# Kernel tuning notes

Measured on AMD Instinct MI355X. Metric: run time of the kernel, lower is better.

## Reference

```python
import jax, jax.numpy as jnp
import numpy as np

B, T, F, U, L, C = 1024, 100, 300, 512, 2, 10
EPS = 1e-3  # keras LayerNormalization default epsilon


def _ln(z, g, b):
    m = jnp.mean(z, axis=-1, keepdims=True)
    v = jnp.var(z, axis=-1, keepdims=True)
    return (z - m) * jax.lax.rsqrt(v + EPS) * g + b


def _cell(xt, h, c, W, R, bias, kg, kb, rg, rb, sg, sb):
    # LayerNormLSTMCell: LN(x@W) + LN(h@R) + b, gates i,f,g,o; LN on new cell state
    z = _ln(xt @ W, kg, kb) + _ln(h @ R, rg, rb) + bias
    i, f, g, o = jnp.split(z, 4, axis=-1)
    c_new = jax.nn.sigmoid(f) * c + jax.nn.sigmoid(i) * jnp.tanh(g)
    c_new = _ln(c_new, sg, sb)
    h_new = jax.nn.sigmoid(o) * jnp.tanh(c_new)
    return h_new, c_new


def setup_inputs() -> dict:
    key = jax.random.key(0)
    ks = jax.random.split(key, 8 + 2 * L)
    d = {}
    d["x"] = jax.random.normal(ks[0], (B, T, F), jnp.float32)
    lens = jax.random.randint(ks[1], (B,), 1, T + 1)
    d["mask"] = (jnp.arange(T)[None, :] < lens[:, None]).astype(jnp.int32)
    in_dims = [F, U]
    ki = 2
    for l in range(L):
        s = 1.0 / np.sqrt(in_dims[l])
        d[f"W{l}"] = jax.random.uniform(ks[ki], (in_dims[l], 4 * U), jnp.float32, -s, s); ki += 1
        d[f"R{l}"] = jax.random.uniform(ks[ki], (U, 4 * U), jnp.float32, -0.044, 0.044); ki += 1
        d[f"b{l}"] = jnp.zeros((4 * U,), jnp.float32)
        d[f"kg{l}"] = jnp.ones((4 * U,), jnp.float32)
        d[f"kb{l}"] = jnp.zeros((4 * U,), jnp.float32)
        d[f"rg{l}"] = jnp.ones((4 * U,), jnp.float32)
        d[f"rb{l}"] = jnp.zeros((4 * U,), jnp.float32)
        d[f"sg{l}"] = jnp.ones((U,), jnp.float32)
        d[f"sb{l}"] = jnp.zeros((U,), jnp.float32)
    s = 1.0 / np.sqrt(U)
    d["Wd"] = jax.random.uniform(ks[ki], (U, C), jnp.float32, -s, s)
    d["bd"] = jnp.zeros((C,), jnp.float32)
    return d


def _forward(x, mask,
             W0, R0, b0, kg0, kb0, rg0, rb0, sg0, sb0,
             W1, R1, b1, kg1, kb1, rg1, rb1, sg1, sb1,
             Wd, bd):
    params = [
        (W0, R0, b0, kg0, kb0, rg0, rb0, sg0, sb0),
        (W1, R1, b1, kg1, kb1, rg1, rb1, sg1, sb1),
    ]
    bsz = x.shape[0]
    dt = x.dtype

    def step(carry, inp_t):
        states, out_prev = carry
        xt, mt = inp_t  # xt: [B,F], mt: [B] bool
        mb = mt[:, None]
        inp = xt
        new_states = []
        for (h, c), p in zip(states, params):
            hn, cn = _cell(inp, h, c, *p)
            inp = hn
            # Keras RNN masking: carry previous state at masked steps
            new_states.append((jnp.where(mb, hn, h), jnp.where(mb, cn, c)))
        out = jnp.where(mb, inp, out_prev)
        return (tuple(new_states), out), None

    init_states = tuple((jnp.zeros((bsz, U), dt), jnp.zeros((bsz, U), dt)) for _ in range(L))
    carry0 = (init_states, jnp.zeros((bsz, U), dt))
    xs = (jnp.transpose(x, (1, 0, 2)), mask.T.astype(bool))  # time-major
    (_, out), _ = jax.lax.scan(step, carry0, xs)
    return jax.nn.softmax(out @ Wd + bd, axis=-1)


def reference(x, mask,
              W0, R0, b0, kg0, kb0, rg0, rb0, sg0, sb0,
              W1, R1, b1, kg1, kb1, rg1, rb1, sg1, sb1,
              Wd, bd):
    return _forward(x, mask,
                    W0, R0, b0, kg0, kb0, rg0, rb0, sg0, sb0,
                    W1, R1, b1, kg1, kb1, rg1, rb1, sg1, sb1,
                    Wd, bd)
```

## Files before the change

kernel.cpp:

```cpp
#include <hip/hip_runtime.h>

#define B_ 1024
#define T_ 100
#define F_ 300
#define FP_ 320
#define U_ 512
#define G4_ 2048
#define C_ 10
#define EPS_ 1e-3f

typedef _Float16 f16x8 __attribute__((ext_vector_type(8)));
typedef float f32x4 __attribute__((ext_vector_type(4)));

typedef __attribute__((address_space(1))) const void* gcptr_t;
typedef __attribute__((address_space(3))) void* lptr_t;

__device__ __forceinline__ void async_ld16(_Float16* lds, const _Float16* g) {
  __builtin_amdgcn_global_load_lds((gcptr_t)g, (lptr_t)lds, 16, 0, 0);
}

__global__ __launch_bounds__(1024) void prep_kernel(const int* __restrict__ mask,
                                                    int* __restrict__ perm,
                                                    int* __restrict__ nt) {
  __shared__ int cnt[T_ + 1];
  __shared__ int start[T_ + 1];
  int b = threadIdx.x;
  if (b <= T_) cnt[b] = 0;
  __syncthreads();
  const int* mrow = mask + (size_t)b * T_;
  int len = 0;
  for (int t = 0; t < T_; t++) len += mrow[t];
  atomicAdd(&cnt[len], 1);
  __syncthreads();
  if (b == 0) {
    int run = 0;
    for (int l = T_; l >= 0; l--) {
      start[l] = run;
      run += cnt[l];
    }
  }
  __syncthreads();
  if (b < T_) nt[b] = start[b];
  __syncthreads();
  int pos = atomicAdd(&start[len], 1);
  perm[pos] = b;
}


__global__ __launch_bounds__(256) void cast_x_kernel(const float* __restrict__ x,
                                                     const int* __restrict__ perm,
                                                     const int* __restrict__ nt,
                                                     _Float16* __restrict__ xhi,
                                                     _Float16* __restrict__ xlo) {
  size_t cidx = (size_t)blockIdx.x * 256 + threadIdx.x;
  int fc = (int)(cidx % (FP_ / 8));
  size_t bt = cidx / (FP_ / 8);
  int i = (int)(bt % B_);
  int t = (int)(bt / B_);
  int nr = (nt[t] + 127) & ~127;
  if (i >= nr) return;
  int b = perm[i];
  int f = fc * 8;
  const float* xr = x + ((size_t)b * T_ + t) * F_;
  float v[8];
  if (f + 8 <= F_) {
    float4 a = *(const float4*)(xr + f);
    float4 c = *(const float4*)(xr + f + 4);
    v[0] = a.x; v[1] = a.y; v[2] = a.z; v[3] = a.w;
    v[4] = c.x; v[5] = c.y; v[6] = c.z; v[7] = c.w;
  } else {
#pragma unroll
    for (int j = 0; j < 8; j++) v[j] = (f + j < F_) ? xr[f + j] : 0.f;
  }
  f16x8 hi, lo;
#pragma unroll
  for (int j = 0; j < 8; j++) {
    _Float16 h = (_Float16)v[j];
    hi[j] = h;
    lo[j] = (_Float16)(v[j] - (float)h);
  }
  *(f16x8*)(xhi + cidx * 8) = hi;
  *(f16x8*)(xlo + cidx * 8) = lo;
}

__global__ __launch_bounds__(256) void cast_w_kernel(const float* __restrict__ W,
                                                     _Float16* __restrict__ Whi,
                                                     _Float16* __restrict__ Wlo,
                                                     int K, int N, int Kp) {
  __shared__ float tile[32][33];
  int n0 = blockIdx.x * 32, k0 = blockIdx.y * 32;
  int tx = threadIdx.x & 31, ty = threadIdx.x >> 5;
#pragma unroll
  for (int r = 0; r < 32; r += 8) {
    int k = k0 + ty + r;
    tile[ty + r][tx] = (k < K) ? W[(size_t)k * N + n0 + tx] : 0.f;
  }
  __syncthreads();
#pragma unroll
  for (int r = 0; r < 32; r += 8) {
    int n = n0 + ty + r, kk = k0 + tx;
    if (kk < Kp) {
      float v = tile[tx][ty + r];
      _Float16 h = (_Float16)v;
      Whi[(size_t)n * Kp + kk] = h;
      Wlo[(size_t)n * Kp + kk] = (_Float16)(v - (float)h);
    }
  }
}

struct GemmOp {
  const _Float16* A;
  const _Float16* Bt;
  float* G;
  int lda;
  int K;
  size_t aLo;
  int step;
};
struct G4Pack {
  GemmOp op[4];
  const int* nt;
};

__global__ __launch_bounds__(512, 1) void gemm_phase(G4Pack P) {
  GemmOp op = P.op[blockIdx.z];
  const int mBase = blockIdx.y * 128, nBase = blockIdx.x * 128;
  if (mBase >= P.nt[op.step]) return;
  const int K = op.K, lda = op.lda;
  const _Float16* Ah = op.A;
  const _Float16* Al = op.A + op.aLo;
  const _Float16* Bh = op.Bt;
  const _Float16* Bl = op.Bt + (size_t)G4_ * K;

  __shared__ __align__(16) _Float16 lds[2][4][128 * 64];

  const int tid = threadIdx.x;
  const int w = tid >> 6;
  const int lane = tid & 63;
  const int wm = (w & 1) << 6;
  const int wn = (w >> 1) << 5;

  f32x4 acc[4][2];
#pragma unroll
  for (int mt = 0; mt < 4; mt++)
#pragma unroll
    for (int nt2 = 0; nt2 < 2; nt2++) acc[mt][nt2] = (f32x4){0.f, 0.f, 0.f, 0.f};

  const int i0 = w << 1;

#define STAGE(BUF, K0)                                                    \
  do {                                                                    \
    _Float16* base_ = &lds[BUF][0][0];                                    \
    _Pragma("unroll") for (int j = 0; j < 2; j++) {                       \
      int i = i0 + j;                                                     \
      int idx = (i << 6) + lane;                                          \
      int row = idx >> 3;                                                 \
      int cl = ((idx & 7) ^ (row & 7)) << 3;                              \
      size_t aoff = (size_t)(mBase + row) * lda + (K0) + cl;              \
      size_t boff = (size_t)(nBase + row) * K + (K0) + cl;                \
      async_ld16(base_ + (i << 9), Ah + aoff);                            \
      async_ld16(base_ + 8192 + (i << 9), Al + aoff);                     \
      async_ld16(base_ + 16384 + (i << 9), Bh + boff);                    \
      async_ld16(base_ + 24576 + (i << 9), Bl + boff);                    \
    }                                                                     \
  } while (0)

  STAGE(0, 0);
  __syncthreads();

  const int nch = K >> 6;
  int cur = 0;
#pragma unroll 1
  for (int c = 0; c < nch; c++) {
    if (c + 1 < nch) STAGE(cur ^ 1, (c + 1) << 6);
    const _Float16* ash = &lds[cur][0][0];
    const _Float16* asl = &lds[cur][1][0];
    const _Float16* bsh = &lds[cur][2][0];
    const _Float16* bsl = &lds[cur][3][0];
#pragma unroll
    for (int q = 0; q < 2; q++) {
      f16x8 afh[4], afl[4], bfh[2], bfl[2];
#pragma unroll
      for (int mt = 0; mt < 4; mt++) {
        int row = wm + (mt << 4) + (lane & 15);
        int p = ((q << 2) + (lane >> 4)) ^ (row & 7);
        afh[mt] = *(const f16x8*)&ash[(row << 6) + (p << 3)];
        afl[mt] = *(const f16x8*)&asl[(row << 6) + (p << 3)];
      }
#pragma unroll
      for (int nt2 = 0; nt2 < 2; nt2++) {
        int row = wn + (nt2 << 4) + (lane & 15);
        int p = ((q << 2) + (lane >> 4)) ^ (row & 7);
        bfh[nt2] = *(const f16x8*)&bsh[(row << 6) + (p << 3)];
        bfl[nt2] = *(const f16x8*)&bsl[(row << 6) + (p << 3)];
      }
      __builtin_amdgcn_s_setprio(1);
#pragma unroll
      for (int mt = 0; mt < 4; mt++)
#pragma unroll
        for (int nt2 = 0; nt2 < 2; nt2++) {
          acc[mt][nt2] = __builtin_amdgcn_mfma_f32_16x16x32_f16(afh[mt], bfh[nt2], acc[mt][nt2], 0, 0, 0);
          acc[mt][nt2] = __builtin_amdgcn_mfma_f32_16x16x32_f16(afl[mt], bfh[nt2], acc[mt][nt2], 0, 0, 0);
          acc[mt][nt2] = __builtin_amdgcn_mfma_f32_16x16x32_f16(afh[mt], bfl[nt2], acc[mt][nt2], 0, 0, 0);
        }
      __builtin_amdgcn_s_setprio(0);
    }
    __syncthreads();
    cur ^= 1;
  }
#undef STAGE

  int q4 = lane >> 4, cc = lane & 15;
  float* G = op.G;
#pragma unroll
  for (int mt = 0; mt < 4; mt++)
#pragma unroll
    for (int nt2 = 0; nt2 < 2; nt2++)
#pragma unroll
      for (int r = 0; r < 4; r++) {
        int row = mBase + wm + (mt << 4) + (q4 << 2) + r;
        int col = nBase + wn + (nt2 << 4) + cc;
        G[(size_t)row * G4_ + col] = acc[mt][nt2][r];
      }
}


__device__ __forceinline__ void block_reduce(float* v, int n, float* sred, int tid) {
  int lane = tid & 63, w = tid >> 6;
  for (int off = 32; off > 0; off >>= 1)
    for (int i = 0; i < n; i++) v[i] += __shfl_down(v[i], off, 64);
  if (lane == 0)
    for (int i = 0; i < n; i++) sred[w * 4 + i] = v[i];
  __syncthreads();
  if (tid == 0)
    for (int i = 0; i < n; i++) sred[16 + i] = sred[i] + sred[4 + i] + sred[8 + i] + sred[12 + i];
  __syncthreads();
  for (int i = 0; i < n; i++) v[i] = sred[16 + i];
}

__device__ __forceinline__ float sigm(float x) { return 1.f / (1.f + expf(-x)); }

struct CellOp {
  const float* Gx;
  const float* Gh;
  const float* bias;
  const float* kg;
  const float* kb;
  const float* rg;
  const float* rb;
  const float* sg;
  const float* sb;
  float* cS;
  _Float16* hP;
  float* outb;
  int step;
};
struct C2Pack {
  CellOp op[2];
  const int* nt;
};

__global__ __launch_bounds__(256) void cell_phase(C2Pack P) {
  CellOp cp = P.op[blockIdx.x >> 10];
  int b = blockIdx.x & (B_ - 1);
  if (b >= P.nt[cp.step]) return;
  int tid = threadIdx.x;
  __shared__ float sred[20];
  const float* gx = cp.Gx + (size_t)b * G4_;
  const float* gh = cp.Gh + (size_t)b * G4_;
  float vx[8], vh[8];
  float s[4] = {0.f, 0.f, 0.f, 0.f};
#pragma unroll
  for (int i = 0; i < 8; i++) {
    int col = tid + (i << 8);
    float a = gx[col], d = gh[col];
    vx[i] = a;
    vh[i] = d;
    s[0] += a;
    s[1] += a * a;
    s[2] += d;
    s[3] += d * d;
  }
  block_reduce(s, 4, sred, tid);
  const float inv = 1.f / 2048.f;
  float m1 = s[0] * inv, m2 = s[2] * inv;
  float rs1 = rsqrtf(fmaxf(s[1] * inv - m1 * m1, 0.f) + EPS_);
  float rs2 = rsqrtf(fmaxf(s[3] * inv - m2 * m2, 0.f) + EPS_);
  float z[8];
#pragma unroll
  for (int i = 0; i < 8; i++) {
    int col = tid + (i << 8);
    z[i] = (vx[i] - m1) * rs1 * cp.kg[col] + cp.kb[col] +
           (vh[i] - m2) * rs2 * cp.rg[col] + cp.rb[col] + cp.bias[col];
  }
  int j0 = tid, j1 = tid + 256;
  size_t base = (size_t)b * U_;
  _Float16* hHi = cp.hP;
  _Float16* hLo = cp.hP + (size_t)B_ * U_;
  float co0 = cp.cS[base + j0], co1 = cp.cS[base + j1];
  float cn0 = sigm(z[2]) * co0 + sigm(z[0]) * tanhf(z[4]);
  float cn1 = sigm(z[3]) * co1 + sigm(z[1]) * tanhf(z[5]);
  float t2[2] = {cn0 + cn1, cn0 * cn0 + cn1 * cn1};
  block_reduce(t2, 2, sred, tid);
  const float invU = 1.f / 512.f;
  float mc = t2[0] * invU;
  float rsc = rsqrtf(fmaxf(t2[1] * invU - mc * mc, 0.f) + EPS_);
  float cl0 = (cn0 - mc) * rsc * cp.sg[j0] + cp.sb[j0];
  float cl1 = (cn1 - mc) * rsc * cp.sg[j1] + cp.sb[j1];
  float hn0 = sigm(z[6]) * tanhf(cl0);
  float hn1 = sigm(z[7]) * tanhf(cl1);
  _Float16 hh0 = (_Float16)hn0, hh1 = (_Float16)hn1;
  hHi[base + j0] = hh0;
  hLo[base + j0] = (_Float16)(hn0 - (float)hh0);
  hHi[base + j1] = hh1;
  hLo[base + j1] = (_Float16)(hn1 - (float)hh1);
  cp.cS[base + j0] = cl0;
  cp.cS[base + j1] = cl1;
  if (cp.outb) {
    cp.outb[base + j0] = hn0;
    cp.outb[base + j1] = hn1;
  }
}

__global__ __launch_bounds__(64) void dense_softmax_kernel(const float* __restrict__ outb,
                                                           const float* __restrict__ Wd,
                                                           const float* __restrict__ bd,
                                                           const int* __restrict__ perm,
                                                           float* __restrict__ o) {
  int b = blockIdx.x, lane = threadIdx.x;
  __shared__ float sl[16];
  int col = lane & 15, kg = lane >> 4;
  float acc = 0.f;
  if (col < C_) {
    for (int k = kg; k < U_; k += 4) acc += outb[(size_t)b * U_ + k] * Wd[(size_t)k * C_ + col];
  }
  acc += __shfl_down(acc, 16, 64);
  acc += __shfl_down(acc, 32, 64);
  if (lane < C_) sl[lane] = acc + bd[lane];
  __syncthreads();
  if (lane < C_) {
    float mx = sl[0];
    for (int i = 1; i < C_; i++) mx = fmaxf(mx, sl[i]);
    float ssum = 0.f;
    for (int i = 0; i < C_; i++) ssum += expf(sl[i] - mx);
    o[(size_t)perm[b] * C_ + lane] = expf(sl[lane] - mx) / ssum;
  }
}


extern "C" void kernel_launch(void* const* d_in, const int* in_sizes, int n_in,
                              void* d_out, int out_size, void* d_ws, size_t ws_size,
                              hipStream_t stream) {
  const float* x = (const float*)d_in[0];
  const int* mask = (const int*)d_in[1];
  const float* W0 = (const float*)d_in[2];
  const float* R0 = (const float*)d_in[3];
  const float* b0 = (const float*)d_in[4];
  const float* kg0 = (const float*)d_in[5];
  const float* kb0 = (const float*)d_in[6];
  const float* rg0 = (const float*)d_in[7];
  const float* rb0 = (const float*)d_in[8];
  const float* sg0 = (const float*)d_in[9];
  const float* sb0 = (const float*)d_in[10];
  const float* W1 = (const float*)d_in[11];
  const float* R1 = (const float*)d_in[12];
  const float* b1 = (const float*)d_in[13];
  const float* kg1 = (const float*)d_in[14];
  const float* kb1 = (const float*)d_in[15];
  const float* rg1 = (const float*)d_in[16];
  const float* rb1 = (const float*)d_in[17];
  const float* sg1 = (const float*)d_in[18];
  const float* sb1 = (const float*)d_in[19];
  const float* Wd = (const float*)d_in[20];
  const float* bd = (const float*)d_in[21];
  float* out = (float*)d_out;

  char* w = (char*)d_ws;
  size_t o = 0;
  auto alloc = [&](size_t bytes) {
    size_t r = o;
    o += (bytes + 255) & ~(size_t)255;
    return r;
  };
  size_t o_c0s = alloc((size_t)B_ * U_ * 4);
  size_t o_c1s = alloc((size_t)B_ * U_ * 4);
  size_t o_outf = alloc((size_t)B_ * U_ * 4);
  size_t o_h0p = alloc((size_t)B_ * U_ * 2 * 2);
  size_t o_h1p = alloc((size_t)B_ * U_ * 2 * 2);
  size_t o_G0h = alloc((size_t)B_ * G4_ * 4);
  size_t zero_bytes = o;
  size_t o_xh = alloc((size_t)T_ * B_ * FP_ * 2 * 2);
  size_t o_W0t = alloc((size_t)G4_ * FP_ * 2 * 2);
  size_t o_R0t = alloc((size_t)G4_ * U_ * 2 * 2);
  size_t o_W1t = alloc((size_t)G4_ * U_ * 2 * 2);
  size_t o_R1t = alloc((size_t)G4_ * U_ * 2 * 2);
  size_t o_G0x = alloc((size_t)B_ * G4_ * 4);
  size_t o_G1x = alloc((size_t)B_ * G4_ * 4);
  size_t o_G1h = alloc((size_t)B_ * G4_ * 4);
  size_t o_perm = alloc((size_t)B_ * 4);
  size_t o_nt = alloc((size_t)T_ * 4);
  (void)ws_size;

  float* c0s = (float*)(w + o_c0s);
  float* c1s = (float*)(w + o_c1s);
  float* outf = (float*)(w + o_outf);
  _Float16* h0p = (_Float16*)(w + o_h0p);
  _Float16* h1p = (_Float16*)(w + o_h1p);
  float* G0h = (float*)(w + o_G0h);
  _Float16* xh = (_Float16*)(w + o_xh);
  _Float16* W0t = (_Float16*)(w + o_W0t);
  _Float16* R0t = (_Float16*)(w + o_R0t);
  _Float16* W1t = (_Float16*)(w + o_W1t);
  _Float16* R1t = (_Float16*)(w + o_R1t);
  float* G0x = (float*)(w + o_G0x);
  float* G1x = (float*)(w + o_G1x);
  float* G1h = (float*)(w + o_G1h);
  int* perm = (int*)(w + o_perm);
  int* ntp = (int*)(w + o_nt);

  hipMemsetAsync(w, 0, zero_bytes, stream);

  prep_kernel<<<1, 1024, 0, stream>>>(mask, perm, ntp);

  {
    size_t chunks = (size_t)T_ * B_ * (FP_ / 8);
    cast_x_kernel<<<dim3((unsigned)(chunks / 256)), 256, 0, stream>>>(
        x, perm, ntp, xh, xh + (size_t)T_ * B_ * FP_);
  }
  cast_w_kernel<<<dim3(G4_ / 32, FP_ / 32), 256, 0, stream>>>(
      W0, W0t, W0t + (size_t)G4_ * FP_, F_, G4_, FP_);
  cast_w_kernel<<<dim3(G4_ / 32, U_ / 32), 256, 0, stream>>>(
      R0, R0t, R0t + (size_t)G4_ * U_, U_, G4_, U_);
  cast_w_kernel<<<dim3(G4_ / 32, U_ / 32), 256, 0, stream>>>(
      W1, W1t, W1t + (size_t)G4_ * U_, U_, G4_, U_);
  cast_w_kernel<<<dim3(G4_ / 32, U_ / 32), 256, 0, stream>>>(
      R1, R1t, R1t + (size_t)G4_ * U_, U_, G4_, U_);

  const size_t xLoOff = (size_t)T_ * B_ * FP_;
  const size_t hLoOff = (size_t)B_ * U_;

  auto xw_op = [&](int t) -> GemmOp {
    return GemmOp{xh + (size_t)t * B_ * FP_, W0t, G0x, FP_, FP_, xLoOff, t};
  };
  CellOp cell0op = {G0x, G0h, b0, kg0, kb0, rg0, rb0, sg0, sb0,
                    c0s, h0p, nullptr, 0};
  CellOp cell1op = {G1x, G1h, b1, kg1, kb1, rg1, rb1, sg1, sb1,
                    c1s, h1p, outf, 0};

  {
    G4Pack P;
    P.nt = ntp;
    P.op[0] = xw_op(0);
    P.op[1] = P.op[0];
    P.op[2] = P.op[0];
    P.op[3] = P.op[0];
    gemm_phase<<<dim3(G4_ / 128, B_ / 128, 1), 512, 0, stream>>>(P);
    C2Pack CP;
    CP.nt = ntp;
    cell0op.step = 0;
    CP.op[0] = cell0op;
    CP.op[1] = cell0op;
    cell_phase<<<B_, 256, 0, stream>>>(CP);
  }

  for (int t = 0; t < T_; t++) {
    bool more = (t < T_ - 1);
    G4Pack P;
    P.nt = ntp;
    P.op[0] = GemmOp{h0p, W1t, G1x, U_, U_, hLoOff, t};
    P.op[1] = GemmOp{h1p, R1t, G1h, U_, U_, hLoOff, t};
    if (more) {
      P.op[2] = GemmOp{h0p, R0t, G0h, U_, U_, hLoOff, t + 1};
      P.op[3] = xw_op(t + 1);
    } else {
      P.op[2] = P.op[0];
      P.op[3] = P.op[0];
    }
    gemm_phase<<<dim3(G4_ / 128, B_ / 128, more ? 4 : 2), 512, 0, stream>>>(P);

    C2Pack CP;
    CP.nt = ntp;
    cell1op.step = t;
    CP.op[0] = cell1op;
    cell0op.step = t + 1;
    CP.op[1] = more ? cell0op : cell1op;
    cell_phase<<<more ? 2 * B_ : B_, 256, 0, stream>>>(CP);
  }

  dense_softmax_kernel<<<B_, 64, 0, stream>>>(outf, Wd, bd, perm, out);
}
```

Before: 3.397 ms.

## Fuse per-step GEMM and cell launches into one persistent cooperative kernel

Replaces the roughly 200 separate gemm_phase and cell_phase launches with a single cooperative kernel of 256 persistent blocks. Each block loops over timesteps, takes GEMM tiles and cell rows in a grid-stride pattern, and uses grid.sync between phases. Tile counts are derived from the sorted active-row counts, so only live tiles are scheduled and no blocks launch just to exit early. The cell computation moves to 512 threads per row to match the block size. In exchange it adds two grid-wide barriers per step and gives up launch-level concurrency.

```diff
diff --git a/kernel.cpp b/kernel.cpp
--- a/kernel.cpp
+++ b/kernel.cpp
@@ -1,4 +1,7 @@
 #include <hip/hip_runtime.h>
+#include <hip/hip_cooperative_groups.h>
+
+namespace cg = cooperative_groups;
 
 #define B_ 1024
 #define T_ 100
@@ -108,37 +111,32 @@
   }
 }
 
-struct GemmOp {
-  const _Float16* A;
-  const _Float16* Bt;
-  float* G;
-  int lda;
-  int K;
-  size_t aLo;
-  int step;
+
+struct CellP {
+  const float *Gx, *Gh, *bias, *kg, *kb, *rg, *rb, *sg, *sb;
+  float* cS;
+  _Float16* hP;
+  float* outb;
 };
-struct G4Pack {
-  GemmOp op[4];
+struct FusedP {
+  const _Float16 *xh, *W0t, *R0t, *W1t, *R1t, *h0pc, *h1pc;
+  float *G0x, *G0h, *G1x, *G1h;
   const int* nt;
+  CellP c0, c1;
 };
 
-__global__ __launch_bounds__(512, 1) void gemm_phase(G4Pack P) {
-  GemmOp op = P.op[blockIdx.z];
-  const int mBase = blockIdx.y * 128, nBase = blockIdx.x * 128;
-  if (mBase >= P.nt[op.step]) return;
-  const int K = op.K, lda = op.lda;
-  const _Float16* Ah = op.A;
-  const _Float16* Al = op.A + op.aLo;
-  const _Float16* Bh = op.Bt;
-  const _Float16* Bl = op.Bt + (size_t)G4_ * K;
-
-  __shared__ __align__(16) _Float16 lds[2][4][128 * 64];
-
-  const int tid = threadIdx.x;
+__device__ __forceinline__ void gemm_tile(const _Float16* __restrict__ Ah,
+                                          const _Float16* __restrict__ Al,
+                                          const _Float16* __restrict__ Bh,
+                                          const _Float16* __restrict__ Bl,
+                                          float* __restrict__ G, int lda, int K,
+                                          int mBase, int nBase, _Float16* lds,
+                                          int tid) {
   const int w = tid >> 6;
   const int lane = tid & 63;
   const int wm = (w & 1) << 6;
   const int wn = (w >> 1) << 5;
+  const int i0 = w << 1;
 
   f32x4 acc[4][2];
 #pragma unroll
@@ -146,37 +144,35 @@
 #pragma unroll
     for (int nt2 = 0; nt2 < 2; nt2++) acc[mt][nt2] = (f32x4){0.f, 0.f, 0.f, 0.f};
 
-  const int i0 = w << 1;
-
-#define STAGE(BUF, K0)                                                    \
-  do {                                                                    \
-    _Float16* base_ = &lds[BUF][0][0];                                    \
-    _Pragma("unroll") for (int j = 0; j < 2; j++) {                       \
-      int i = i0 + j;                                                     \
-      int idx = (i << 6) + lane;                                          \
-      int row = idx >> 3;                                                 \
-      int cl = ((idx & 7) ^ (row & 7)) << 3;                              \
-      size_t aoff = (size_t)(mBase + row) * lda + (K0) + cl;              \
-      size_t boff = (size_t)(nBase + row) * K + (K0) + cl;                \
-      async_ld16(base_ + (i << 9), Ah + aoff);                            \
-      async_ld16(base_ + 8192 + (i << 9), Al + aoff);                     \
-      async_ld16(base_ + 16384 + (i << 9), Bh + boff);                    \
-      async_ld16(base_ + 24576 + (i << 9), Bl + boff);                    \
-    }                                                                     \
-  } while (0)
-
-  STAGE(0, 0);
+  auto stage = [&](int buf, int k0) {
+    _Float16* base_ = lds + buf * 32768;
+#pragma unroll
+    for (int j = 0; j < 2; j++) {
+      int i = i0 + j;
+      int idx = (i << 6) + lane;
+      int row = idx >> 3;
+      int cl = ((idx & 7) ^ (row & 7)) << 3;
+      size_t aoff = (size_t)(mBase + row) * lda + k0 + cl;
+      size_t boff = (size_t)(nBase + row) * K + k0 + cl;
+      async_ld16(base_ + (i << 9), Ah + aoff);
+      async_ld16(base_ + 8192 + (i << 9), Al + aoff);
+      async_ld16(base_ + 16384 + (i << 9), Bh + boff);
+      async_ld16(base_ + 24576 + (i << 9), Bl + boff);
+    }
+  };
+
+  stage(0, 0);
   __syncthreads();
 
   const int nch = K >> 6;
   int cur = 0;
 #pragma unroll 1
   for (int c = 0; c < nch; c++) {
-    if (c + 1 < nch) STAGE(cur ^ 1, (c + 1) << 6);
-    const _Float16* ash = &lds[cur][0][0];
-    const _Float16* asl = &lds[cur][1][0];
-    const _Float16* bsh = &lds[cur][2][0];
-    const _Float16* bsl = &lds[cur][3][0];
+    if (c + 1 < nch) stage(cur ^ 1, (c + 1) << 6);
+    const _Float16* ash = lds + cur * 32768;
+    const _Float16* asl = ash + 8192;
+    const _Float16* bsh = ash + 16384;
+    const _Float16* bsl = ash + 24576;
 #pragma unroll
     for (int q = 0; q < 2; q++) {
       f16x8 afh[4], afl[4], bfh[2], bfl[2];
@@ -208,10 +204,8 @@
     __syncthreads();
     cur ^= 1;
   }
-#undef STAGE
 
   int q4 = lane >> 4, cc = lane & 15;
-  float* G = op.G;
 #pragma unroll
   for (int mt = 0; mt < 4; mt++)
 #pragma unroll
@@ -224,55 +218,35 @@
       }
 }
 
-
-__device__ __forceinline__ void block_reduce(float* v, int n, float* sred, int tid) {
-  int lane = tid & 63, w = tid >> 6;
+__device__ __forceinline__ void block_reduce8(float* v, int n, float (*sred)[4], int tid) {
+  int lane = tid & 63, wv = tid >> 6;
   for (int off = 32; off > 0; off >>= 1)
     for (int i = 0; i < n; i++) v[i] += __shfl_down(v[i], off, 64);
   if (lane == 0)
-    for (int i = 0; i < n; i++) sred[w * 4 + i] = v[i];
-  __syncthreads();
-  if (tid == 0)
-    for (int i = 0; i < n; i++) sred[16 + i] = sred[i] + sred[4 + i] + sred[8 + i] + sred[12 + i];
-  __syncthreads();
-  for (int i = 0; i < n; i++) v[i] = sred[16 + i];
+    for (int i = 0; i < n; i++) sred[wv][i] = v[i];
+  __syncthreads();
+  if (tid == 0) {
+    for (int i = 0; i < n; i++) {
+      float a = 0.f;
+      for (int k2 = 0; k2 < 8; k2++) a += sred[k2][i];
+      sred[8][i] = a;
+    }
+  }
+  __syncthreads();
+  for (int i = 0; i < n; i++) v[i] = sred[8][i];
 }
 
 __device__ __forceinline__ float sigm(float x) { return 1.f / (1.f + expf(-x)); }
 
-struct CellOp {
-  const float* Gx;
-  const float* Gh;
-  const float* bias;
-  const float* kg;
-  const float* kb;
-  const float* rg;
-  const float* rb;
-  const float* sg;
-  const float* sb;
-  float* cS;
-  _Float16* hP;
-  float* outb;
-  int step;
-};
-struct C2Pack {
-  CellOp op[2];
-  const int* nt;
-};
-
-__global__ __launch_bounds__(256) void cell_phase(C2Pack P) {
-  CellOp cp = P.op[blockIdx.x >> 10];
-  int b = blockIdx.x & (B_ - 1);
-  if (b >= P.nt[cp.step]) return;
-  int tid = threadIdx.x;
-  __shared__ float sred[20];
-  const float* gx = cp.Gx + (size_t)b * G4_;
-  const float* gh = cp.Gh + (size_t)b * G4_;
-  float vx[8], vh[8];
+__device__ __forceinline__ void do_cell(const CellP& cp, int row, int tid,
+                                        float (*sred)[4]) {
+  const float* gx = cp.Gx + (size_t)row * G4_;
+  const float* gh = cp.Gh + (size_t)row * G4_;
+  float vx[4], vh[4];
   float s[4] = {0.f, 0.f, 0.f, 0.f};
 #pragma unroll
-  for (int i = 0; i < 8; i++) {
-    int col = tid + (i << 8);
+  for (int i = 0; i < 4; i++) {
+    int col = tid + (i << 9);
     float a = gx[col], d = gh[col];
     vx[i] = a;
     vh[i] = d;
@@ -281,44 +255,98 @@
     s[2] += d;
     s[3] += d * d;
   }
-  block_reduce(s, 4, sred, tid);
+  block_reduce8(s, 4, sred, tid);
   const float inv = 1.f / 2048.f;
   float m1 = s[0] * inv, m2 = s[2] * inv;
   float rs1 = rsqrtf(fmaxf(s[1] * inv - m1 * m1, 0.f) + EPS_);
   float rs2 = rsqrtf(fmaxf(s[3] * inv - m2 * m2, 0.f) + EPS_);
-  float z[8];
-#pragma unroll
-  for (int i = 0; i < 8; i++) {
-    int col = tid + (i << 8);
+  float z[4];
+#pragma unroll
+  for (int i = 0; i < 4; i++) {
+    int col = tid + (i << 9);
     z[i] = (vx[i] - m1) * rs1 * cp.kg[col] + cp.kb[col] +
            (vh[i] - m2) * rs2 * cp.rg[col] + cp.rb[col] + cp.bias[col];
   }
-  int j0 = tid, j1 = tid + 256;
-  size_t base = (size_t)b * U_;
-  _Float16* hHi = cp.hP;
-  _Float16* hLo = cp.hP + (size_t)B_ * U_;
-  float co0 = cp.cS[base + j0], co1 = cp.cS[base + j1];
-  float cn0 = sigm(z[2]) * co0 + sigm(z[0]) * tanhf(z[4]);
-  float cn1 = sigm(z[3]) * co1 + sigm(z[1]) * tanhf(z[5]);
-  float t2[2] = {cn0 + cn1, cn0 * cn0 + cn1 * cn1};
-  block_reduce(t2, 2, sred, tid);
+  size_t base = (size_t)row * U_ + tid;
+  float co = cp.cS[base];
+  float cn = sigm(z[1]) * co + sigm(z[0]) * tanhf(z[2]);
+  float t2[4] = {cn, cn * cn, 0.f, 0.f};
+  block_reduce8(t2, 2, sred, tid);
   const float invU = 1.f / 512.f;
   float mc = t2[0] * invU;
   float rsc = rsqrtf(fmaxf(t2[1] * invU - mc * mc, 0.f) + EPS_);
-  float cl0 = (cn0 - mc) * rsc * cp.sg[j0] + cp.sb[j0];
-  float cl1 = (cn1 - mc) * rsc * cp.sg[j1] + cp.sb[j1];
-  float hn0 = sigm(z[6]) * tanhf(cl0);
-  float hn1 = sigm(z[7]) * tanhf(cl1);
-  _Float16 hh0 = (_Float16)hn0, hh1 = (_Float16)hn1;
-  hHi[base + j0] = hh0;
-  hLo[base + j0] = (_Float16)(hn0 - (float)hh0);
-  hHi[base + j1] = hh1;
-  hLo[base + j1] = (_Float16)(hn1 - (float)hh1);
-  cp.cS[base + j0] = cl0;
-  cp.cS[base + j1] = cl1;
-  if (cp.outb) {
-    cp.outb[base + j0] = hn0;
-    cp.outb[base + j1] = hn1;
+  float cl = (cn - mc) * rsc * cp.sg[tid] + cp.sb[tid];
+  float hn = sigm(z[3]) * tanhf(cl);
+  _Float16 hh = (_Float16)hn;
+  cp.hP[base] = hh;
+  cp.hP[base + (size_t)B_ * U_] = (_Float16)(hn - (float)hh);
+  cp.cS[base] = cl;
+  if (cp.outb) cp.outb[base] = hn;
+}
+
+__global__ __launch_bounds__(512, 1) void fused_rnn_kernel(FusedP P) {
+  cg::grid_group grid = cg::this_grid();
+  __shared__ __align__(16) _Float16 lds[2][4][8192];
+  __shared__ float sred[9][4];
+  _Float16* ldsp = &lds[0][0][0];
+  const int tid = threadIdx.x;
+  const int bid = blockIdx.x;
+  const int nbk = gridDim.x;
+  const int* nt = P.nt;
+
+  const size_t hLo = (size_t)B_ * U_;
+  const size_t xLo = (size_t)T_ * B_ * FP_;
+  const size_t wLoU = (size_t)G4_ * U_;
+  const size_t wLoF = (size_t)G4_ * FP_;
+
+#pragma unroll 1
+  for (int t = -1; t < T_; t++) {
+    const bool more = (t < T_ - 1);
+    const int nt0 = (t >= 0) ? nt[t] : 0;
+    const int nt1 = more ? nt[t + 1] : 0;
+    const int mb0 = (nt0 + 127) >> 7;
+    const int mb1 = (nt1 + 127) >> 7;
+    const int s0 = mb0 << 4;
+    const int s01 = s0 << 1;
+    const int nOp2 = (t >= 0 && more) ? (mb1 << 4) : 0;
+    const int nOp3 = more ? (mb1 << 4) : 0;
+    const int ntile = s01 + nOp2 + nOp3;
+
+    for (int tl = bid; tl < ntile; tl += nbk) {
+      int op, rem;
+      if (tl < s0) { op = 0; rem = tl; }
+      else if (tl < s01) { op = 1; rem = tl - s0; }
+      else if (tl < s01 + nOp2) { op = 2; rem = tl - s01; }
+      else { op = 3; rem = tl - s01 - nOp2; }
+      int m = rem >> 4, n = rem & 15;
+      const _Float16 *Ah, *Al, *Bh, *Bl;
+      float* Gp;
+      int lda, K;
+      if (op == 0) {
+        Ah = P.h0pc; Al = P.h0pc + hLo; Bh = P.W1t; Bl = P.W1t + wLoU;
+        Gp = P.G1x; lda = U_; K = U_;
+      } else if (op == 1) {
+        Ah = P.h1pc; Al = P.h1pc + hLo; Bh = P.R1t; Bl = P.R1t + wLoU;
+        Gp = P.G1h; lda = U_; K = U_;
+      } else if (op == 2) {
+        Ah = P.h0pc; Al = P.h0pc + hLo; Bh = P.R0t; Bl = P.R0t + wLoU;
+        Gp = P.G0h; lda = U_; K = U_;
+      } else {
+        Ah = P.xh + (size_t)(t + 1) * B_ * FP_;
+        Al = Ah + xLo;
+        Bh = P.W0t; Bl = P.W0t + wLoF;
+        Gp = P.G0x; lda = FP_; K = FP_;
+      }
+      gemm_tile(Ah, Al, Bh, Bl, Gp, lda, K, m << 7, n << 7, ldsp, tid);
+    }
+    grid.sync();
+
+    const int total = nt0 + nt1;
+    for (int j = bid; j < total; j += nbk) {
+      if (j < nt0) do_cell(P.c1, j, tid, sred);
+      else do_cell(P.c0, j - nt0, tid, sred);
+    }
+    grid.sync();
   }
 }
 
@@ -436,56 +464,25 @@
   cast_w_kernel<<<dim3(G4_ / 32, U_ / 32), 256, 0, stream>>>(
       R1, R1t, R1t + (size_t)G4_ * U_, U_, G4_, U_);
 
-  const size_t xLoOff = (size_t)T_ * B_ * FP_;
-  const size_t hLoOff = (size_t)B_ * U_;
-
-  auto xw_op = [&](int t) -> GemmOp {
-    return GemmOp{xh + (size_t)t * B_ * FP_, W0t, G0x, FP_, FP_, xLoOff, t};
-  };
-  CellOp cell0op = {G0x, G0h, b0, kg0, kb0, rg0, rb0, sg0, sb0,
-                    c0s, h0p, nullptr, 0};
-  CellOp cell1op = {G1x, G1h, b1, kg1, kb1, rg1, rb1, sg1, sb1,
-                    c1s, h1p, outf, 0};
-
-  {
-    G4Pack P;
-    P.nt = ntp;
-    P.op[0] = xw_op(0);
-    P.op[1] = P.op[0];
-    P.op[2] = P.op[0];
-    P.op[3] = P.op[0];
-    gemm_phase<<<dim3(G4_ / 128, B_ / 128, 1), 512, 0, stream>>>(P);
-    C2Pack CP;
-    CP.nt = ntp;
-    cell0op.step = 0;
-    CP.op[0] = cell0op;
-    CP.op[1] = cell0op;
-    cell_phase<<<B_, 256, 0, stream>>>(CP);
-  }
-
-  for (int t = 0; t < T_; t++) {
-    bool more = (t < T_ - 1);
-    G4Pack P;
-    P.nt = ntp;
-    P.op[0] = GemmOp{h0p, W1t, G1x, U_, U_, hLoOff, t};
-    P.op[1] = GemmOp{h1p, R1t, G1h, U_, U_, hLoOff, t};
-    if (more) {
-      P.op[2] = GemmOp{h0p, R0t, G0h, U_, U_, hLoOff, t + 1};
-      P.op[3] = xw_op(t + 1);
-    } else {
-      P.op[2] = P.op[0];
-      P.op[3] = P.op[0];
-    }
-    gemm_phase<<<dim3(G4_ / 128, B_ / 128, more ? 4 : 2), 512, 0, stream>>>(P);
-
-    C2Pack CP;
-    CP.nt = ntp;
-    cell1op.step = t;
-    CP.op[0] = cell1op;
-    cell0op.step = t + 1;
-    CP.op[1] = more ? cell0op : cell1op;
-    cell_phase<<<more ? 2 * B_ : B_, 256, 0, stream>>>(CP);
-  }
+  FusedP FPk;
+  FPk.xh = xh;
+  FPk.W0t = W0t;
+  FPk.R0t = R0t;
+  FPk.W1t = W1t;
+  FPk.R1t = R1t;
+  FPk.h0pc = h0p;
+  FPk.h1pc = h1p;
+  FPk.G0x = G0x;
+  FPk.G0h = G0h;
+  FPk.G1x = G1x;
+  FPk.G1h = G1h;
+  FPk.nt = ntp;
+  FPk.c0 = CellP{G0x, G0h, b0, kg0, kb0, rg0, rb0, sg0, sb0, c0s, h0p, nullptr};
+  FPk.c1 = CellP{G1x, G1h, b1, kg1, kb1, rg1, rb1, sg1, sb1, c1s, h1p, outf};
+
+  void* kargs[] = {(void*)&FPk};
+  hipLaunchCooperativeKernel((const void*)fused_rnn_kernel, dim3(256), dim3(512),
+                             kargs, 0, stream);
 
   dense_softmax_kernel<<<B_, 64, 0, stream>>>(outf, Wd, bd, perm, out);
 }
```

Result: slower. 10.28 ms (+202.6%).
